# Kernel tuning notes

Measured on AMD Instinct MI355X. Metric: run time of the kernel, lower is better.

Reference implementation:

```python
import jax, jax.numpy as jnp
import numpy as np

T = 96      # CONTEXT_SIZE
B = 32      # BATCH_SIZE
DIN = 256   # input_dim
H = 512     # hidden_dim
V = 128     # output_dim (vocab)


def setup_inputs() -> dict:
    key = jax.random.key(0)
    ks = jax.random.split(key, 16)
    s_in = 1.0 / np.sqrt(DIN)
    s_h = 1.0 / np.sqrt(H)

    def u(k, shape, s):
        return jax.random.uniform(k, shape, jnp.float32, -s, s)

    return {
        "x": jax.random.normal(ks[0], (B, T, DIN), jnp.float32),
        # input->hidden gate weights (no bias), one per timestep: [T, H, DIN]
        "Wif": u(ks[1], (T, H, DIN), s_in),
        "Wii": u(ks[2], (T, H, DIN), s_in),
        "Wic": u(ks[3], (T, H, DIN), s_in),
        "Wio": u(ks[4], (T, H, DIN), s_in),
        # hidden->hidden gate weights (+bias), one per timestep: [T, H, H], [T, H]
        "Whf_w": u(ks[5], (T, H, H), s_h), "Whf_b": u(ks[6], (T, H), s_h),
        "Whi_w": u(ks[7], (T, H, H), s_h), "Whi_b": u(ks[8], (T, H), s_h),
        "Whc_w": u(ks[9], (T, H, H), s_h), "Whc_b": u(ks[10], (T, H), s_h),
        "Who_w": u(ks[11], (T, H, H), s_h), "Who_b": u(ks[12], (T, H), s_h),
        # per-step output projections: [T, V, H], [T, V]
        "lin_w": u(ks[13], (T, V, H), s_h), "lin_b": u(ks[14], (T, V), s_h),
    }


def reference(x, Wif, Wii, Wic, Wio, Whf_w, Whf_b, Whi_w, Whi_b,
              Whc_w, Whc_b, Who_w, Who_b, lin_w, lin_b):
    sig = jax.nn.sigmoid

    # --- step 0: h_prev/c_prev are None -> hidden-path linears (and their
    # biases) are entirely absent, and c_t = i * c_bar (no forget term).
    x0 = x[:, 0]                                    # [B, DIN]
    i0 = sig(x0 @ Wii[0].T)
    cb0 = jnp.tanh(x0 @ Wic[0].T)
    o0 = sig(x0 @ Wio[0].T)
    c0 = i0 * cb0
    h0 = o0 * jnp.tanh(c0)                          # [B, H]
    logit0 = h0 @ lin_w[0].T + lin_b[0]             # [B, V]

    # --- steps 1..T-1: full gated update, distinct weights per step.
    def step(carry, ws):
        c, h = carry
        (xt, wif, whfw, whfb, wii, whiw, whib,
         wic, whcw, whcb, wio, whow, whob, lw, lb) = ws
        f = sig(xt @ wif.T + h @ whfw.T + whfb)
        i = sig(xt @ wii.T + h @ whiw.T + whib)
        cb = jnp.tanh(xt @ wic.T + h @ whcw.T + whcb)
        o = sig(xt @ wio.T + h @ whow.T + whob)
        c_t = f * c + i * cb
        h_t = o * jnp.tanh(c_t)
        return (c_t, h_t), h_t @ lw.T + lb

    xs = (jnp.swapaxes(x, 0, 1)[1:],               # [T-1, B, DIN]
          Wif[1:], Whf_w[1:], Whf_b[1:],
          Wii[1:], Whi_w[1:], Whi_b[1:],
          Wic[1:], Whc_w[1:], Whc_b[1:],
          Wio[1:], Who_w[1:], Who_b[1:],
          lin_w[1:], lin_b[1:])
    _, logits_rest = jax.lax.scan(step, (c0, h0), xs)   # [T-1, B, V]

    logits = jnp.concatenate([logit0[None], logits_rest], axis=0)  # [T, B, V]
    # original stacks [B, 1, V] per step along dim=1 -> [B, T, 1, V]
    return jnp.transpose(logits, (1, 0, 2))[:, :, None, :]
```

## Files before the change

### kernel.cpp

```cpp
#include <hip/hip_runtime.h>
#include <hip/hip_bf16.h>

#define TT 96
#define BB 32
#define DIN 256
#define HH 512
#define VV 128
#define NB 256

__global__ __launch_bounds__(256) void phaseA_kernel(
    const float* __restrict__ x,
    const float* __restrict__ Wf, const float* __restrict__ Wi,
    const float* __restrict__ Wc, const float* __restrict__ Wo,
    float* __restrict__ Z)
{
    int bid  = blockIdx.x;
    int t    = bid >> 4;
    int tile = bid & 15;
    int g    = tile >> 2;
    int h0   = (tile & 3) * 128;
    const float* W = (g == 0) ? Wf : (g == 1) ? Wi : (g == 2) ? Wc : Wo;

    __shared__ float4 Xs4[32 * 64];
    __shared__ float4 Wc4[128 * 8];

    int tid = threadIdx.x;
    {
        int b   = tid >> 3;
        int kq8 = tid & 7;
        const float* src = x + ((size_t)b * TT + t) * DIN;
        int bx = b & 15;
        #pragma unroll
        for (int j = 0; j < 8; ++j) {
            int q = kq8 * 8 + j;
            Xs4[b * 64 + (q ^ bx)] = *reinterpret_cast<const float4*>(src + q * 4);
        }
    }

    int rg = tid >> 3;
    int bg = tid & 7;
    const float* wbase = W + ((size_t)t * HH + h0) * DIN;

    int srow[4], sgq[4];
    #pragma unroll
    for (int j = 0; j < 4; ++j) {
        int s = j * 256 + tid;
        srow[j] = s >> 3;
        sgq[j]  = (s & 7) ^ ((srow[j] >> 2) & 7);
    }

    float4 stg[4];
    #pragma unroll
    for (int j = 0; j < 4; ++j)
        stg[j] = *reinterpret_cast<const float4*>(wbase + (size_t)srow[j] * DIN + sgq[j] * 4);

    float acc[4][4];
    #pragma unroll
    for (int r = 0; r < 4; ++r)
        #pragma unroll
        for (int c = 0; c < 4; ++c) acc[r][c] = 0.f;

    for (int kc = 0; kc < 8; ++kc) {
        __syncthreads();
        #pragma unroll
        for (int j = 0; j < 4; ++j) Wc4[j * 256 + tid] = stg[j];
        __syncthreads();
        if (kc < 7) {
            #pragma unroll
            for (int j = 0; j < 4; ++j)
                stg[j] = *reinterpret_cast<const float4*>(
                    wbase + (size_t)srow[j] * DIN + (kc + 1) * 32 + sgq[j] * 4);
        }
        #pragma unroll
        for (int q = 0; q < 8; ++q) {
            float4 xv[4], wv[4];
            #pragma unroll
            for (int c = 0; c < 4; ++c) {
                int b = c * 8 + bg;
                xv[c] = Xs4[b * 64 + ((kc * 8 + q) ^ (b & 15))];
            }
            #pragma unroll
            for (int r = 0; r < 4; ++r)
                wv[r] = Wc4[(rg * 4 + r) * 8 + (q ^ (rg & 7))];
            #pragma unroll
            for (int r = 0; r < 4; ++r)
                #pragma unroll
                for (int c = 0; c < 4; ++c) {
                    acc[r][c] = fmaf(wv[r].x, xv[c].x, acc[r][c]);
                    acc[r][c] = fmaf(wv[r].y, xv[c].y, acc[r][c]);
                    acc[r][c] = fmaf(wv[r].z, xv[c].z, acc[r][c]);
                    acc[r][c] = fmaf(wv[r].w, xv[c].w, acc[r][c]);
                }
        }
    }

    size_t zbase = ((size_t)(t * 4 + g) * HH + h0 + rg * 4) * BB;
    #pragma unroll
    for (int r = 0; r < 4; ++r)
        #pragma unroll
        for (int c = 0; c < 4; ++c)
            Z[zbase + (size_t)r * BB + c * 8 + bg] = acc[r][c];
}

__global__ __launch_bounds__(512, 2) void lstm_persistent(
    const float* __restrict__ Whf, const float* __restrict__ Whi,
    const float* __restrict__ Whc, const float* __restrict__ Who,
    const float* __restrict__ bf,  const float* __restrict__ bi,
    const float* __restrict__ bc,  const float* __restrict__ bo,
    const float* __restrict__ Z,   float* __restrict__ Hall,
    unsigned* __restrict__ bar)
{
    int blk = blockIdx.x;
    int r0  = blk * 2;
    int gid = blk >> 4;
    int tid = threadIdx.x;
    int ks  = tid >> 4;
    int bg  = tid & 15;

    __shared__ float pre[32][8][32];
    __shared__ float act[8][32];

    float creg = 0.f;

    for (int t = 0; t < TT; ++t) {
        float4 pfw0, pfw1, pfw2;
        float4 pfz;
        float  pfb;
        bool pf_on = (t + 1 < TT) && (tid >= 64);
        int  idx   = tid - 64;
        if (pf_on) {
            #pragma unroll
            for (int j = 0; j < 2; ++j) {
                int f    = idx + j * 448;
                int gate = f >> 8;
                int rl   = (f >> 7) & 1;
                int q    = f & 127;
                const float* wsrc = ((gate == 0) ? Whf : (gate == 1) ? Whi :
                                     (gate == 2) ? Whc : Who)
                                    + ((size_t)(t + 1) * HH + r0 + rl) * HH + q * 4;
                float4 v = *reinterpret_cast<const float4*>(wsrc);
                if (j == 0) pfw0 = v; else pfw1 = v;
            }
            if (idx < 128) {
                int f    = idx + 896;
                int gate = f >> 8;
                int rl   = (f >> 7) & 1;
                int q    = f & 127;
                const float* wsrc = ((gate == 0) ? Whf : (gate == 1) ? Whi :
                                     (gate == 2) ? Whc : Who)
                                    + ((size_t)(t + 1) * HH + r0 + rl) * HH + q * 4;
                pfw2 = *reinterpret_cast<const float4*>(wsrc);
            }
            if (idx < 64) {
                int g2 = idx >> 4, rl = (idx >> 3) & 1, qq = idx & 7;
                pfz = *reinterpret_cast<const float4*>(
                    Z + ((size_t)((t + 1) * 4 + g2) * HH + r0 + rl) * BB + qq * 4);
            }
            if (idx < 8) {
                int g2 = idx >> 1, rl = idx & 1;
                const float* bp = (g2 == 0) ? bf : (g2 == 1) ? bi : (g2 == 2) ? bc : bo;
                pfb = bp[(size_t)(t + 1) * HH + r0 + rl];
            }
        }

        float a[8][2];
        #pragma unroll
        for (int rg = 0; rg < 8; ++rg) { a[rg][0] = 0.f; a[rg][1] = 0.f; }

        if (t > 0) {
            int k0 = ks * 16;
            const float* hbase = Hall + (size_t)(t - 1) * HH * BB + (size_t)k0 * BB + 2 * bg;
            const float* wp[8];
            #pragma unroll
            for (int rl = 0; rl < 2; ++rl) {
                size_t wo = ((size_t)t * HH + r0 + rl) * HH + k0;
                wp[rl * 4 + 0] = Whf + wo;
                wp[rl * 4 + 1] = Whi + wo;
                wp[rl * 4 + 2] = Whc + wo;
                wp[rl * 4 + 3] = Who + wo;
            }
            #pragma unroll
            for (int q = 0; q < 4; ++q) {
                float2 hv[4];
                #pragma unroll
                for (int j = 0; j < 4; ++j)
                    hv[j] = *reinterpret_cast<const float2*>(hbase + (size_t)(q * 4 + j) * BB);
                #pragma unroll
                for (int rg = 0; rg < 8; ++rg) {
                    float4 w = *reinterpret_cast<const float4*>(wp[rg] + q * 4);
                    a[rg][0] = fmaf(w.x, hv[0].x, a[rg][0]); a[rg][1] = fmaf(w.x, hv[0].y, a[rg][1]);
                    a[rg][0] = fmaf(w.y, hv[1].x, a[rg][0]); a[rg][1] = fmaf(w.y, hv[1].y, a[rg][1]);
                    a[rg][0] = fmaf(w.z, hv[2].x, a[rg][0]); a[rg][1] = fmaf(w.z, hv[2].y, a[rg][1]);
                    a[rg][0] = fmaf(w.w, hv[3].x, a[rg][0]); a[rg][1] = fmaf(w.w, hv[3].y, a[rg][1]);
                }
            }
        }
        #pragma unroll
        for (int rg = 0; rg < 8; ++rg) {
            pre[ks][rg][2 * bg]     = a[rg][0];
            pre[ks][rg][2 * bg + 1] = a[rg][1];
        }

        if (pf_on) {
            float s = pfw0.x + pfw0.y + pfw0.z + pfw0.w
                    + pfw1.x + pfw1.y + pfw1.z + pfw1.w;
            if (idx < 128) s += pfw2.x + pfw2.y + pfw2.z + pfw2.w;
            if (idx < 64)  s += pfz.x + pfz.y + pfz.z + pfz.w;
            if (idx < 8)   s += pfb;
            asm volatile("" :: "v"(s));
        }

        __syncthreads();

        if (tid < 256) {
            int rg2 = tid >> 5;
            int b   = tid & 31;
            int row = r0 + (rg2 >> 2);
            int g   = rg2 & 3;
            float s = 0.f;
            #pragma unroll
            for (int k2 = 0; k2 < 32; ++k2) s += pre[k2][rg2][b];
            s += Z[((size_t)(t * 4 + g) * HH + row) * BB + b];
            if (t > 0) {
                const float* bp = (g == 0) ? bf : (g == 1) ? bi : (g == 2) ? bc : bo;
                s += bp[t * HH + row];
            }
            act[rg2][b] = (g == 2) ? tanhf(s) : 1.f / (1.f + __expf(-s));
        }
        __syncthreads();

        if (tid < 64) {
            int rl = tid >> 5, b = tid & 31;
            float cn = act[rl * 4 + 0][b] * creg + act[rl * 4 + 1][b] * act[rl * 4 + 2][b];
            creg = cn;
            float hn = act[rl * 4 + 3][b] * tanhf(cn);
            __hip_atomic_store(Hall + ((size_t)t * HH + r0 + rl) * BB + b, hn,
                               __ATOMIC_RELAXED, __HIP_MEMORY_SCOPE_AGENT);
        }

        if (t + 1 < TT) {
            if (tid < 64)
                asm volatile("s_waitcnt vmcnt(0)" ::: "memory");
            if (tid == 0) {
                unsigned* grp  = bar + ((size_t)t * 32 + gid) * 16;
                unsigned* root = bar + ((size_t)t * 32 + 16) * 16;
                unsigned* flag = bar + ((size_t)t * 32 + 17) * 16;
                unsigned prev = __hip_atomic_fetch_add(grp, 1u, __ATOMIC_RELAXED,
                                                       __HIP_MEMORY_SCOPE_AGENT);
                if (prev == 15u) {
                    unsigned p2 = __hip_atomic_fetch_add(root, 1u, __ATOMIC_RELAXED,
                                                         __HIP_MEMORY_SCOPE_AGENT);
                    if (p2 == 15u)
                        __hip_atomic_store(flag, 1u, __ATOMIC_RELAXED,
                                           __HIP_MEMORY_SCOPE_AGENT);
                }
                while (__hip_atomic_load(flag, __ATOMIC_RELAXED,
                                         __HIP_MEMORY_SCOPE_AGENT) == 0u)
                    __builtin_amdgcn_s_sleep(1);
            }
            __syncthreads();
        }
    }
}

__global__ __launch_bounds__(256) void phaseC_kernel(
    const float* __restrict__ lw, const float* __restrict__ lb,
    const float* __restrict__ Hall, float* __restrict__ out)
{
    int t  = blockIdx.x >> 2;
    int v0 = (blockIdx.x & 3) << 5;
    int tid = threadIdx.x;
    int v  = v0 + (tid >> 3);
    int bg = tid & 7;
    const float* w  = lw + ((size_t)t * VV + v) * HH;
    const float* hp = Hall + (size_t)t * HH * BB;
    float acc0 = 0.f, acc1 = 0.f, acc2 = 0.f, acc3 = 0.f;
    #pragma unroll 4
    for (int k = 0; k < HH; ++k) {
        float wv = w[k];
        float4 hv = *reinterpret_cast<const float4*>(hp + (size_t)k * BB + bg * 4);
        acc0 = fmaf(wv, hv.x, acc0);
        acc1 = fmaf(wv, hv.y, acc1);
        acc2 = fmaf(wv, hv.z, acc2);
        acc3 = fmaf(wv, hv.w, acc3);
    }
    float bias = lb[t * VV + v];
    float r[4] = {acc0 + bias, acc1 + bias, acc2 + bias, acc3 + bias};
    #pragma unroll
    for (int j = 0; j < 4; ++j) {
        int b = bg * 4 + j;
        out[((size_t)b * TT + t) * VV + v] = r[j];
    }
}

extern "C" void kernel_launch(void* const* d_in, const int* in_sizes, int n_in,
                              void* d_out, int out_size, void* d_ws, size_t ws_size,
                              hipStream_t stream)
{
    const float* x     = (const float*)d_in[0];
    const float* Wif   = (const float*)d_in[1];
    const float* Wii   = (const float*)d_in[2];
    const float* Wic   = (const float*)d_in[3];
    const float* Wio   = (const float*)d_in[4];
    const float* Whf_w = (const float*)d_in[5];
    const float* Whf_b = (const float*)d_in[6];
    const float* Whi_w = (const float*)d_in[7];
    const float* Whi_b = (const float*)d_in[8];
    const float* Whc_w = (const float*)d_in[9];
    const float* Whc_b = (const float*)d_in[10];
    const float* Who_w = (const float*)d_in[11];
    const float* Who_b = (const float*)d_in[12];
    const float* lin_w = (const float*)d_in[13];
    const float* lin_b = (const float*)d_in[14];
    float* out = (float*)d_out;

    float*    Z    = (float*)d_ws;
    float*    Hall = Z + (size_t)TT * 4 * HH * BB;
    unsigned* bar  = (unsigned*)(Hall + (size_t)TT * HH * BB);

    hipMemsetAsync(bar, 0, (size_t)TT * 32 * 16 * sizeof(unsigned), stream);

    phaseA_kernel<<<dim3(TT * 16), dim3(256), 0, stream>>>(x, Wif, Wii, Wic, Wio, Z);

    lstm_persistent<<<dim3(NB), dim3(512), 0, stream>>>(
        Whf_w, Whi_w, Whc_w, Who_w, Whf_b, Whi_b, Whc_b, Who_b, Z, Hall, bar);

    phaseC_kernel<<<dim3(TT * 4), dim3(256), 0, stream>>>(lin_w, lin_b, Hall, out);
}
```

Before: 0.9999 ms.

## Replace tree atomic grid barrier with per-block flags polled by a full wavefront

Replaces the two-level atomic counter barrier with per-block monotonic flags. Each block's first wavefront publishes its step and then polls all 256 flags in parallel with 64-bit loads, using a wave-wide vote to detect completion. The prefetch of the next step's weights moves to the upper 256 threads, which consume it after the gate phase. Plain s_barrier with an lgkmcnt wait replaces __syncthreads. This removes the serialized atomic chain and cuts barrier latency on the critical recurrent path, but it raises polling traffic to L2 and relies on relaxed ordering being enough for visibility of Hall.

Result: slower. 1.024 ms (+2.4%).

```diff
diff --git a/kernel.cpp b/kernel.cpp
--- a/kernel.cpp
+++ b/kernel.cpp
@@ -7,6 +7,8 @@
 #define HH 512
 #define VV 128
 #define NB 256
+
+#define BAR() asm volatile("s_waitcnt lgkmcnt(0)\ns_barrier" ::: "memory")
 
 __global__ __launch_bounds__(256) void phaseA_kernel(
     const float* __restrict__ x,
@@ -108,11 +110,10 @@
     const float* __restrict__ bf,  const float* __restrict__ bi,
     const float* __restrict__ bc,  const float* __restrict__ bo,
     const float* __restrict__ Z,   float* __restrict__ Hall,
-    unsigned* __restrict__ bar)
+    unsigned* __restrict__ flags)
 {
     int blk = blockIdx.x;
     int r0  = blk * 2;
-    int gid = blk >> 4;
     int tid = threadIdx.x;
     int ks  = tid >> 4;
     int bg  = tid & 15;
@@ -123,33 +124,22 @@
     float creg = 0.f;
 
     for (int t = 0; t < TT; ++t) {
-        float4 pfw0, pfw1, pfw2;
+        float4 pfw[4];
         float4 pfz;
         float  pfb;
-        bool pf_on = (t + 1 < TT) && (tid >= 64);
-        int  idx   = tid - 64;
+        bool pf_on = (t + 1 < TT) && (tid >= 256);
+        int  idx   = tid - 256;
         if (pf_on) {
             #pragma unroll
-            for (int j = 0; j < 2; ++j) {
-                int f    = idx + j * 448;
+            for (int j = 0; j < 4; ++j) {
+                int f    = j * 256 + idx;
                 int gate = f >> 8;
                 int rl   = (f >> 7) & 1;
                 int q    = f & 127;
                 const float* wsrc = ((gate == 0) ? Whf : (gate == 1) ? Whi :
                                      (gate == 2) ? Whc : Who)
                                     + ((size_t)(t + 1) * HH + r0 + rl) * HH + q * 4;
-                float4 v = *reinterpret_cast<const float4*>(wsrc);
-                if (j == 0) pfw0 = v; else pfw1 = v;
-            }
-            if (idx < 128) {
-                int f    = idx + 896;
-                int gate = f >> 8;
-                int rl   = (f >> 7) & 1;
-                int q    = f & 127;
-                const float* wsrc = ((gate == 0) ? Whf : (gate == 1) ? Whi :
-                                     (gate == 2) ? Whc : Who)
-                                    + ((size_t)(t + 1) * HH + r0 + rl) * HH + q * 4;
-                pfw2 = *reinterpret_cast<const float4*>(wsrc);
+                pfw[j] = *reinterpret_cast<const float4*>(wsrc);
             }
             if (idx < 64) {
                 int g2 = idx >> 4, rl = (idx >> 3) & 1, qq = idx & 7;
@@ -201,16 +191,7 @@
             pre[ks][rg][2 * bg + 1] = a[rg][1];
         }
 
-        if (pf_on) {
-            float s = pfw0.x + pfw0.y + pfw0.z + pfw0.w
-                    + pfw1.x + pfw1.y + pfw1.z + pfw1.w;
-            if (idx < 128) s += pfw2.x + pfw2.y + pfw2.z + pfw2.w;
-            if (idx < 64)  s += pfz.x + pfz.y + pfz.z + pfz.w;
-            if (idx < 8)   s += pfb;
-            asm volatile("" :: "v"(s));
-        }
-
-        __syncthreads();
+        BAR();
 
         if (tid < 256) {
             int rg2 = tid >> 5;
@@ -227,7 +208,8 @@
             }
             act[rg2][b] = (g == 2) ? tanhf(s) : 1.f / (1.f + __expf(-s));
         }
-        __syncthreads();
+
+        BAR();
 
         if (tid < 64) {
             int rl = tid >> 5, b = tid & 31;
@@ -236,30 +218,36 @@
             float hn = act[rl * 4 + 3][b] * tanhf(cn);
             __hip_atomic_store(Hall + ((size_t)t * HH + r0 + rl) * BB + b, hn,
                                __ATOMIC_RELAXED, __HIP_MEMORY_SCOPE_AGENT);
-        }
-
-        if (t + 1 < TT) {
-            if (tid < 64)
+            if (t + 1 < TT) {
                 asm volatile("s_waitcnt vmcnt(0)" ::: "memory");
-            if (tid == 0) {
-                unsigned* grp  = bar + ((size_t)t * 32 + gid) * 16;
-                unsigned* root = bar + ((size_t)t * 32 + 16) * 16;
-                unsigned* flag = bar + ((size_t)t * 32 + 17) * 16;
-                unsigned prev = __hip_atomic_fetch_add(grp, 1u, __ATOMIC_RELAXED,
-                                                       __HIP_MEMORY_SCOPE_AGENT);
-                if (prev == 15u) {
-                    unsigned p2 = __hip_atomic_fetch_add(root, 1u, __ATOMIC_RELAXED,
-                                                         __HIP_MEMORY_SCOPE_AGENT);
-                    if (p2 == 15u)
-                        __hip_atomic_store(flag, 1u, __ATOMIC_RELAXED,
-                                           __HIP_MEMORY_SCOPE_AGENT);
+                if (tid == 0)
+                    __hip_atomic_store(&flags[blk], (unsigned)(t + 1),
+                                       __ATOMIC_RELAXED, __HIP_MEMORY_SCOPE_AGENT);
+                {
+                    const unsigned long long* f64 = (const unsigned long long*)flags;
+                    unsigned long long tv = (unsigned long long)(unsigned)(t + 1);
+                    tv |= tv << 32;
+                    for (;;) {
+                        unsigned long long v0 = __hip_atomic_load(
+                            &f64[tid * 2], __ATOMIC_RELAXED, __HIP_MEMORY_SCOPE_AGENT);
+                        unsigned long long v1 = __hip_atomic_load(
+                            &f64[tid * 2 + 1], __ATOMIC_RELAXED, __HIP_MEMORY_SCOPE_AGENT);
+                        if (__all(v0 == tv && v1 == tv)) break;
+                        __builtin_amdgcn_s_sleep(1);
+                    }
                 }
-                while (__hip_atomic_load(flag, __ATOMIC_RELAXED,
-                                         __HIP_MEMORY_SCOPE_AGENT) == 0u)
-                    __builtin_amdgcn_s_sleep(1);
-            }
-            __syncthreads();
-        }
+            }
+        } else if (pf_on) {
+            float s = pfw[0].x + pfw[0].y + pfw[0].z + pfw[0].w
+                    + pfw[1].x + pfw[1].y + pfw[1].z + pfw[1].w
+                    + pfw[2].x + pfw[2].y + pfw[2].z + pfw[2].w
+                    + pfw[3].x + pfw[3].y + pfw[3].z + pfw[3].w;
+            if (idx < 64) s += pfz.x + pfz.y + pfz.z + pfz.w;
+            if (idx < 8)  s += pfb;
+            asm volatile("" :: "v"(s));
+        }
+
+        BAR();
     }
 }
 
@@ -314,16 +302,16 @@
     const float* lin_b = (const float*)d_in[14];
     float* out = (float*)d_out;
 
-    float*    Z    = (float*)d_ws;
-    float*    Hall = Z + (size_t)TT * 4 * HH * BB;
-    unsigned* bar  = (unsigned*)(Hall + (size_t)TT * HH * BB);
-
-    hipMemsetAsync(bar, 0, (size_t)TT * 32 * 16 * sizeof(unsigned), stream);
+    float*    Z     = (float*)d_ws;
+    float*    Hall  = Z + (size_t)TT * 4 * HH * BB;
+    unsigned* flags = (unsigned*)(Hall + (size_t)TT * HH * BB);
+
+    hipMemsetAsync(flags, 0, NB * sizeof(unsigned), stream);
 
     phaseA_kernel<<<dim3(TT * 16), dim3(256), 0, stream>>>(x, Wif, Wii, Wic, Wio, Z);
 
     lstm_persistent<<<dim3(NB), dim3(512), 0, stream>>>(
-        Whf_w, Whi_w, Whc_w, Who_w, Whf_b, Whi_b, Whc_b, Who_b, Z, Hall, bar);
+        Whf_w, Whi_w, Whc_w, Who_w, Whf_b, Whi_b, Whc_b, Who_b, Z, Hall, flags);
 
     phaseC_kernel<<<dim3(TT * 4), dim3(256), 0, stream>>>(lin_w, lin_b, Hall, out);
 }
```
